# Kernel tuning notes

Measured on AMD Instinct MI355X. Metric: run time of the kernel, lower is better.

## Reference

```python
import jax, jax.numpy as jnp
import numpy as np

F = 26            # number of categorical fields
V_FIELD = 8000    # vocab per field
V = F * V_FIELD   # 208000, size of every shared-index table
D_EMB = 16
DNN_IN = F * F * D_EMB  # 10816
H1, H2 = 256, 128
BS = 4096
NUM_DENSE = 13
EPS = 1e-5


def setup_inputs() -> dict:
    key = jax.random.key(0)
    ks = jax.random.split(key, 16)
    def n(k, shape, s=0.05):
        return jax.random.normal(k, shape, dtype=jnp.float32) * s
    return {
        "X_sparse": jax.random.randint(ks[0], (BS, F), 0, V_FIELD, dtype=jnp.int32),
        "X_dense": jax.random.normal(ks[1], (BS, NUM_DENSE), dtype=jnp.float32),
        "fm1_emb": n(ks[2], (V, 1)),
        "bias": jnp.zeros((1,), jnp.float32),
        "fm1_dense_W": n(ks[3], (1, NUM_DENSE)),
        "fm1_dense_b": jnp.zeros((1,), jnp.float32),
        "emb_tables": n(ks[4], (F, V, D_EMB)),  # one table per field (FFM)
        "dense_W": n(ks[5], (DNN_IN, NUM_DENSE)),
        "dense_b": jnp.zeros((DNN_IN,), jnp.float32),
        "W1": n(ks[6], (H1, DNN_IN)),
        "b1": jnp.zeros((H1,), jnp.float32),
        "g1": jnp.ones((H1,), jnp.float32),
        "beta1": jnp.zeros((H1,), jnp.float32),
        "W2": n(ks[7], (H2, H1)),
        "b2": jnp.zeros((H2,), jnp.float32),
        "g2": jnp.ones((H2,), jnp.float32),
        "beta2": jnp.zeros((H2,), jnp.float32),
        "Wout": n(ks[8], (1, H2)),
        "bout": jnp.zeros((1,), jnp.float32),
    }


def _bn(x, g, b):
    # BatchNorm1d in training mode: biased batch statistics
    m = jnp.mean(x, axis=0)
    v = jnp.var(x, axis=0)
    return (x - m) * jax.lax.rsqrt(v + EPS) * g + b


def reference(X_sparse, X_dense, fm1_emb, bias, fm1_dense_W, fm1_dense_b,
              emb_tables, dense_W, dense_b,
              W1, b1, g1, beta1, W2, b2, g2, beta2, Wout, bout):
    offsets = (jnp.arange(F, dtype=X_sparse.dtype) * V_FIELD)[None, :]
    X = X_sparse + offsets                      # [bs, F] global indices

    # FM first order
    fm1 = jnp.sum(fm1_emb[X], axis=1) + bias    # [bs, 1]
    fm1 = fm1 + X_dense @ fm1_dense_W.T + fm1_dense_b

    # FFM second order: E[t, b, f, d] = table t looked up at field f's index
    E = emb_tables[:, X, :]                     # [F, bs, F, d]
    A = jnp.transpose(E, (1, 0, 2, 3))          # [bs, F_table, F_field, d]
    # pair (i<j): xs[j][:, i] * xs[i][:, j] = A[b, i, j] * A[b, j, i]
    P = A * jnp.swapaxes(A, 1, 2)               # [bs, F, F, d]
    mask = jnp.triu(jnp.ones((F, F), jnp.float32), 1)
    fm2 = jnp.einsum('bijd,ij->b', P, mask)[:, None]  # [bs, 1]

    # DNN: concat per-table lookups then flatten -> [bs, F*F*d]
    dnn = A.reshape(A.shape[0], DNN_IN)
    dnn = dnn + jax.nn.relu(X_dense @ dense_W.T + dense_b)
    h = jax.nn.relu(_bn(dnn @ W1.T + b1, g1, beta1))  # dropout is identity (eval)
    h = jax.nn.relu(_bn(h @ W2.T + b2, g2, beta2))
    out = h @ Wout.T + bout
    return jax.nn.sigmoid(fm1 + fm2 + out)
```

## Files before the change

### kernel.cpp

```cpp
#include <hip/hip_runtime.h>

typedef __bf16 bf16x8 __attribute__((ext_vector_type(8)));
typedef float f32x4 __attribute__((ext_vector_type(4)));

#define F_FIELDS 26
#define V_FIELD  8000
#define V_TOT    208000
#define D_EMBD   16
#define DNN_IN   10816
#define BS       4096
#define ND       13
#define H1_DIM   256
#define H2_DIM   128
#define NP1      8

__device__ __forceinline__ unsigned short f2bf(float f) {
  unsigned u = __float_as_uint(f);
  u += 0x7fffu + ((u >> 16) & 1u);
  return (unsigned short)(u >> 16);
}
__device__ __forceinline__ float bf2f(unsigned short h) {
  return __uint_as_float(((unsigned)h) << 16);
}
__device__ __forceinline__ float bflo(unsigned u) { return __uint_as_float(u << 16); }
__device__ __forceinline__ float bfhi(unsigned u) { return __uint_as_float(u & 0xffff0000u); }

__device__ __forceinline__ void gload16(const void* g, void* l) {
  __builtin_amdgcn_global_load_lds(
      (const __attribute__((address_space(1))) unsigned int*)g,
      (__attribute__((address_space(3))) unsigned int*)l, 16, 0, 0);
}

__device__ __forceinline__ float dot8bf(uint4 a, uint4 b) {
  const unsigned* pa = (const unsigned*)&a;
  const unsigned* pb = (const unsigned*)&b;
  float s = 0.f;
#pragma unroll
  for (int k = 0; k < 4; ++k)
    s += bflo(pa[k]) * bflo(pb[k]) + bfhi(pa[k]) * bfhi(pb[k]);
  return s;
}

__global__ __launch_bounds__(256) void k_gather(
    const int* __restrict__ Xs, const float* __restrict__ emb,
    const float* __restrict__ fm1_emb, const float* __restrict__ bias,
    const float* __restrict__ fm1dW, const float* __restrict__ fm1db,
    const float* __restrict__ Xd,
    const float* __restrict__ W1, const float* __restrict__ W2,
    const float* __restrict__ dW, const float* __restrict__ db_,
    unsigned short* __restrict__ W1b, unsigned short* __restrict__ W2b,
    unsigned short* __restrict__ dWb,
    unsigned short* __restrict__ Abf, float* __restrict__ fm12) {
  const int b = blockIdx.x;
  const int tid = threadIdx.x;
  const int lane = tid & 63, wave = tid >> 6;
  __shared__ int   sidx[F_FIELDS];
  __shared__ float sc1[F_FIELDS];
  __shared__ __align__(16) unsigned short As[676 * 16];
  __shared__ float wred[4];

  if (tid < F_FIELDS) {
    int v = Xs[b * F_FIELDS + tid] + tid * V_FIELD;
    sidx[tid] = v;
    sc1[tid] = fm1_emb[v];
  }
  __syncthreads();

  const int q = tid & 3, rbase = tid >> 2;
  float4 vv[11];
#pragma unroll
  for (int it = 0; it < 11; ++it) {
    int r = rbase + it * 64;
    if (r < 676) {
      int i = r / 26, j = r - i * 26;
      const float* src = emb + ((size_t)i * V_TOT + sidx[j]) * D_EMBD + q * 4;
      vv[it] = *(const float4*)src;
    }
  }
  const int n1 = H1_DIM * DNN_IN, n2 = H2_DIM * H1_DIM;
  for (int t = b * 256 + tid; t < n1 + n2; t += BS * 256) {
    if (t < n1) W1b[t] = f2bf(W1[t]);
    else        W2b[t - n1] = f2bf(W2[t - n1]);
  }
  for (int e = b * 256 + tid; e < DNN_IN; e += BS * 256) {
    unsigned short row[32];
#pragma unroll
    for (int k = 0; k < 13; ++k) row[k] = f2bf(dW[e * 13 + k]);
    row[13] = f2bf(db_[e]);
#pragma unroll
    for (int k = 14; k < 32; ++k) row[k] = 0;
#pragma unroll
    for (int k = 0; k < 32; ++k) dWb[e * 32 + k] = row[k];
  }
#pragma unroll
  for (int it = 0; it < 11; ++it) {
    int r = rbase + it * 64;
    if (r < 676) {
      ushort4 u;
      u.x = f2bf(vv[it].x); u.y = f2bf(vv[it].y);
      u.z = f2bf(vv[it].z); u.w = f2bf(vv[it].w);
      *(ushort4*)&As[r * 16 + q * 4] = u;
      *(ushort4*)&Abf[(size_t)b * DNN_IN + r * 16 + q * 4] = u;
    }
  }
  __syncthreads();

  float acc2 = 0.f;
  for (int p = tid; p < 325; p += 256) {
    float disc = sqrtf((float)(2601 - 8 * p));
    int i = (int)((51.f - disc) * 0.5f);
    int cum = 25 * i - ((i * (i - 1)) >> 1);
    int j = i + 1 + (p - cum);
    const unsigned short* r1 = &As[(i * 26 + j) * 16];
    const unsigned short* r2 = &As[(j * 26 + i) * 16];
    acc2 += dot8bf(*(const uint4*)r1, *(const uint4*)r2);
    acc2 += dot8bf(*(const uint4*)(r1 + 8), *(const uint4*)(r2 + 8));
  }
#pragma unroll
  for (int off = 32; off; off >>= 1) acc2 += __shfl_down(acc2, off);
  if (lane == 0) wred[wave] = acc2;
  __syncthreads();
  if (tid == 0) {
    float fm2 = wred[0] + wred[1] + wred[2] + wred[3];
    float f1 = bias[0] + fm1db[0];
#pragma unroll
    for (int j = 0; j < F_FIELDS; ++j) f1 += sc1[j];
    for (int k = 0; k < ND; ++k) f1 += Xd[b * ND + k] * fm1dW[k];
    fm12[b] = f1 + fm2;
  }
}

__global__ __launch_bounds__(256) void k_gemm1(
    const unsigned short* __restrict__ A, const unsigned short* __restrict__ B,
    const unsigned short* __restrict__ dWb, const float* __restrict__ Xd,
    float* __restrict__ C) {
  __shared__ __align__(16) unsigned short sA[3][64 * 32];
  __shared__ __align__(16) unsigned short sB[3][256 * 32];
  __shared__ __align__(16) unsigned short sWd[3][1024];
  __shared__ __align__(16) unsigned short sD[64 * 32];
  __shared__ __align__(16) unsigned short sXd[64 * 32];
  const int tid = threadIdx.x;
  const int lane = tid & 63, w = tid >> 6;
  const int id = blockIdx.x;
  const int p = id & 7, mt = id >> 3;
  const int m0 = mt * 64;
  const int s0 = (338 * p) >> 3, s1 = (338 * (p + 1)) >> 3;
  C += (size_t)p * ((size_t)BS * H1_DIM);

  if (tid < 64) {
    const float* xr = Xd + (size_t)(m0 + tid) * ND;
    unsigned short row[32];
#pragma unroll
    for (int k = 0; k < 13; ++k) row[k] = f2bf(xr[k]);
    row[13] = 0x3F80;
#pragma unroll
    for (int k = 14; k < 32; ++k) row[k] = 0;
#pragma unroll
    for (int k = 0; k < 32; ++k) sXd[tid * 32 + k] = row[k];
  }
  __syncthreads();

  const int q = tid & 3, rr = tid >> 2;
  const unsigned short* gA  = A + (size_t)(m0 + rr) * DNN_IN + q * 8;
  const unsigned short* gB0 = B + (size_t)rr * DNN_IN + q * 8;
  const int fr = lane & 15, fk = lane >> 4;
  const int oA = fr * 32 + fk * 8;
  const int oB = (w * 64 + fr) * 32 + fk * 8;

  const bf16x8 avd = *(const bf16x8*)&sXd[(w * 16 + fr) * 32 + fk * 8];
  const int oW0 = fr * 32 + fk * 8;
  const int oW1 = (16 + fr) * 32 + fk * 8;
  const int drow = w * 16 + fk * 4;

  f32x4 acc[4][4] = {};
  const f32x4 zf = {0.f, 0.f, 0.f, 0.f};

#define STAGE1(ks, bi) do { const int ko_ = (ks) * 32;                      \
    gload16(gA + ko_, &sA[bi][tid * 8]);                                    \
    gload16(gB0 + ko_, &sB[bi][tid * 8]);                                   \
    gload16(gB0 + (size_t)64 * DNN_IN + ko_, &sB[bi][2048 + tid * 8]);      \
    gload16(gB0 + (size_t)128 * DNN_IN + ko_, &sB[bi][4096 + tid * 8]);     \
    gload16(gB0 + (size_t)192 * DNN_IN + ko_, &sB[bi][6144 + tid * 8]);     \
    gload16(dWb + (size_t)ko_ * 32 + (size_t)lane * 8, &sWd[bi][lane * 8]); \
    gload16(dWb + (size_t)ko_ * 32 + 512 + (size_t)lane * 8,                \
            &sWd[bi][512 + lane * 8]); } while (0)

  STAGE1(s0, 0);
  if (s0 + 1 < s1) STAGE1(s0 + 1, 1);
  if (s0 + 2 < s1) STAGE1(s0 + 2, 2);

  int bi = 0;
  for (int ks = s0; ks < s1; ++ks) {
    if (ks + 2 < s1)      asm volatile("s_waitcnt vmcnt(14)" ::: "memory");
    else if (ks + 1 < s1) asm volatile("s_waitcnt vmcnt(7)" ::: "memory");
    else                  asm volatile("s_waitcnt vmcnt(0)" ::: "memory");
    __builtin_amdgcn_sched_barrier(0);
    __builtin_amdgcn_s_barrier();
    bf16x8 bw0 = *(const bf16x8*)&sWd[bi][oW0];
    bf16x8 bw1 = *(const bf16x8*)&sWd[bi][oW1];
    bf16x8 av[4], bv[4];
#pragma unroll
    for (int mi = 0; mi < 4; ++mi) av[mi] = *(const bf16x8*)&sA[bi][oA + mi * 512];
#pragma unroll
    for (int ni = 0; ni < 4; ++ni) bv[ni] = *(const bf16x8*)&sB[bi][oB + ni * 512];
    asm volatile("s_waitcnt lgkmcnt(0)" ::: "memory");
    __builtin_amdgcn_sched_barrier(0);
    f32x4 d0 = __builtin_amdgcn_mfma_f32_16x16x32_bf16(avd, bw0, zf, 0, 0, 0);
    f32x4 d1 = __builtin_amdgcn_mfma_f32_16x16x32_bf16(avd, bw1, zf, 0, 0, 0);
#pragma unroll
    for (int mi = 0; mi < 4; ++mi)
#pragma unroll
      for (int ni = 0; ni < 4; ++ni)
        acc[mi][ni] = __builtin_amdgcn_mfma_f32_16x16x32_bf16(
            av[mi], bv[ni], acc[mi][ni], 0, 0, 0);
#pragma unroll
    for (int r = 0; r < 4; ++r) {
      sD[(drow + r) * 32 + fr]      = f2bf(fmaxf(d0[r], 0.f));
      sD[(drow + r) * 32 + 16 + fr] = f2bf(fmaxf(d1[r], 0.f));
    }
    asm volatile("s_waitcnt lgkmcnt(0)" ::: "memory");
    __builtin_amdgcn_sched_barrier(0);
    __builtin_amdgcn_s_barrier();
    if (ks + 3 < s1) STAGE1(ks + 3, bi);
    bf16x8 dv[4];
#pragma unroll
    for (int mi = 0; mi < 4; ++mi) dv[mi] = *(const bf16x8*)&sD[oA + mi * 512];
    asm volatile("s_waitcnt lgkmcnt(0)" ::: "memory");
    __builtin_amdgcn_sched_barrier(0);
#pragma unroll
    for (int mi = 0; mi < 4; ++mi)
#pragma unroll
      for (int ni = 0; ni < 4; ++ni)
        acc[mi][ni] = __builtin_amdgcn_mfma_f32_16x16x32_bf16(
            dv[mi], bv[ni], acc[mi][ni], 0, 0, 0);
    bi = bi + 1; if (bi == 3) bi = 0;
  }
#pragma unroll
  for (int mi = 0; mi < 4; ++mi)
#pragma unroll
    for (int ni = 0; ni < 4; ++ni)
#pragma unroll
      for (int r = 0; r < 4; ++r) {
        int row = m0 + mi * 16 + fk * 4 + r;
        int col = w * 64 + ni * 16 + fr;
        C[(size_t)row * H1_DIM + col] = acc[mi][ni][r];
      }
#undef STAGE1
}

__global__ __launch_bounds__(256) void k_stat1(
    const float* __restrict__ Yp, const float* __restrict__ b1,
    float* __restrict__ Y1, float* __restrict__ ps, float* __restrict__ pq) {
  const int g = blockIdx.x, n = threadIdx.x;
  const size_t plane = (size_t)BS * H1_DIM;
  float s = 0.f, s2 = 0.f;
  float bn = b1[n];
  for (int bb = 0; bb < 16; ++bb) {
    size_t o = (size_t)(g * 16 + bb) * H1_DIM + n;
    float y = bn;
#pragma unroll
    for (int pp = 0; pp < NP1; ++pp) y += Yp[o + pp * plane];
    Y1[o] = y; s += y; s2 += y * y;
  }
  ps[g * H1_DIM + n] = s;
  pq[g * H1_DIM + n] = s2;
}

__global__ __launch_bounds__(256) void k_apply1(
    const float* __restrict__ Y1, const float* __restrict__ ps,
    const float* __restrict__ pq, const float* __restrict__ g1,
    const float* __restrict__ be1, unsigned short* __restrict__ H1b) {
  const int g = blockIdx.x, n = threadIdx.x;
  float s = 0.f, s2 = 0.f;
  for (int gg = 0; gg < 256; ++gg) {
    s += ps[gg * H1_DIM + n];
    s2 += pq[gg * H1_DIM + n];
  }
  float m = s * (1.f / BS);
  float v = s2 * (1.f / BS) - m * m;
  float r = rsqrtf(v + 1e-5f);
  float ga = g1[n], bb_ = be1[n];
  for (int bb = 0; bb < 16; ++bb) {
    size_t o = (size_t)(g * 16 + bb) * H1_DIM + n;
    float h = (Y1[o] - m) * r * ga + bb_;
    H1b[o] = f2bf(fmaxf(h, 0.f));
  }
}

__global__ __launch_bounds__(256) void k_gemm2(
    const unsigned short* __restrict__ A, const unsigned short* __restrict__ B,
    const float* __restrict__ b2, float* __restrict__ Y2,
    float* __restrict__ ps, float* __restrict__ pq) {
  __shared__ __align__(16) unsigned short sA[2][128 * 32];
  __shared__ __align__(16) unsigned short sB[2][128 * 32];
  __shared__ float redS[8][H2_DIM];
  __shared__ float redQ[8][H2_DIM];
  const int tid = threadIdx.x;
  const int lane = tid & 63, wave = tid >> 6;
  const int m0 = blockIdx.x * 128;

  const int q = tid & 3, rr = tid >> 2;
  const unsigned short* gA0 = A + (size_t)(m0 + rr) * H1_DIM + q * 8;
  const unsigned short* gA1 = gA0 + (size_t)64 * H1_DIM;
  const unsigned short* gB0 = B + (size_t)rr * H1_DIM + q * 8;
  const unsigned short* gB1 = gB0 + (size_t)64 * H1_DIM;
  const int lo = wave * 512;

  const int wr = wave >> 1, wc = wave & 1;
  const int fr = lane & 15, fk = lane >> 4;
  const int oA = (wr * 64 + fr) * 32 + fk * 8;
  const int oB = (wc * 64 + fr) * 32 + fk * 8;

  f32x4 acc[4][4] = {};
  {
    gload16(gA0, &sA[0][lo]);
    gload16(gA1, &sA[0][2048 + lo]);
    gload16(gB0, &sB[0][lo]);
    gload16(gB1, &sB[0][2048 + lo]);
  }
  for (int ks = 0; ks < 8; ++ks) {
    const int cur = ks & 1;
    if (ks + 1 < 8) {
      const int ko = (ks + 1) * 32;
      gload16(gA0 + ko, &sA[cur ^ 1][lo]);
      gload16(gA1 + ko, &sA[cur ^ 1][2048 + lo]);
      gload16(gB0 + ko, &sB[cur ^ 1][lo]);
      gload16(gB1 + ko, &sB[cur ^ 1][2048 + lo]);
      asm volatile("s_waitcnt vmcnt(4)" ::: "memory");
    } else {
      asm volatile("s_waitcnt vmcnt(0)" ::: "memory");
    }
    __builtin_amdgcn_sched_barrier(0);
    __builtin_amdgcn_s_barrier();
    bf16x8 av[4], bv[4];
#pragma unroll
    for (int mi = 0; mi < 4; ++mi) av[mi] = *(const bf16x8*)&sA[cur][oA + mi * 512];
#pragma unroll
    for (int ni = 0; ni < 4; ++ni) bv[ni] = *(const bf16x8*)&sB[cur][oB + ni * 512];
    asm volatile("s_waitcnt lgkmcnt(0)" ::: "memory");
    __builtin_amdgcn_sched_barrier(0);
    __builtin_amdgcn_s_barrier();
#pragma unroll
    for (int mi = 0; mi < 4; ++mi)
#pragma unroll
      for (int ni = 0; ni < 4; ++ni)
        acc[mi][ni] = __builtin_amdgcn_mfma_f32_16x16x32_bf16(
            av[mi], bv[ni], acc[mi][ni], 0, 0, 0);
  }
  float sc[4] = {0.f, 0.f, 0.f, 0.f}, sq[4] = {0.f, 0.f, 0.f, 0.f};
#pragma unroll
  for (int ni = 0; ni < 4; ++ni) {
    int col = wc * 64 + ni * 16 + fr;
    float bcol = b2[col];
#pragma unroll
    for (int mi = 0; mi < 4; ++mi)
#pragma unroll
      for (int r = 0; r < 4; ++r) {
        int row = m0 + wr * 64 + mi * 16 + fk * 4 + r;
        float y = acc[mi][ni][r] + bcol;
        Y2[(size_t)row * H2_DIM + col] = y;
        sc[ni] += y; sq[ni] += y * y;
      }
  }
  const int slot = wr * 4 + fk;
#pragma unroll
  for (int ni = 0; ni < 4; ++ni) {
    int col = wc * 64 + ni * 16 + fr;
    redS[slot][col] = sc[ni];
    redQ[slot][col] = sq[ni];
  }
  __syncthreads();
  if (tid < H2_DIM) {
    float s = 0.f, s2 = 0.f;
#pragma unroll
    for (int sl = 0; sl < 8; ++sl) { s += redS[sl][tid]; s2 += redQ[sl][tid]; }
    ps[blockIdx.x * H2_DIM + tid] = s;
    pq[blockIdx.x * H2_DIM + tid] = s2;
  }
}

__global__ __launch_bounds__(256) void k_final(
    const float* __restrict__ Y2, const float* __restrict__ ps,
    const float* __restrict__ pq, const float* __restrict__ g2,
    const float* __restrict__ be2, const float* __restrict__ Wout,
    const float* __restrict__ bout, const float* __restrict__ fm12,
    float* __restrict__ out) {
  const int tid = threadIdx.x, wave = tid >> 6, lane = tid & 63;
  __shared__ float sm[H2_DIM], sr[H2_DIM], sg[H2_DIM], sbe[H2_DIM], sw[H2_DIM];
  if (tid < H2_DIM) {
    float s = 0.f, s2 = 0.f;
    for (int g = 0; g < 32; ++g) {
      s += ps[g * H2_DIM + tid];
      s2 += pq[g * H2_DIM + tid];
    }
    float m = s * (1.f / BS);
    float v = s2 * (1.f / BS) - m * m;
    sm[tid] = m; sr[tid] = rsqrtf(v + 1e-5f);
    sg[tid] = g2[tid]; sbe[tid] = be2[tid]; sw[tid] = Wout[tid];
  }
  __syncthreads();
  const float bo = bout[0];
  for (int ii = 0; ii < 16; ++ii) {
    int s = blockIdx.x * 64 + wave * 16 + ii;
    float acc = 0.f;
#pragma unroll
    for (int nn = 0; nn < 2; ++nn) {
      int n = lane + nn * 64;
      float y = Y2[(size_t)s * H2_DIM + n];
      float h = (y - sm[n]) * sr[n] * sg[n] + sbe[n];
      acc += fmaxf(h, 0.f) * sw[n];
    }
#pragma unroll
    for (int off = 32; off; off >>= 1) acc += __shfl_down(acc, off);
    if (lane == 0) {
      float logit = fm12[s] + acc + bo;
      out[s] = 1.f / (1.f + expf(-logit));
    }
  }
}

extern "C" void kernel_launch(void* const* d_in, const int* in_sizes, int n_in,
                              void* d_out, int out_size, void* d_ws, size_t ws_size,
                              hipStream_t stream) {
  const int*   Xs     = (const int*)d_in[0];
  const float* Xd     = (const float*)d_in[1];
  const float* fm1e   = (const float*)d_in[2];
  const float* bias   = (const float*)d_in[3];
  const float* fm1dW  = (const float*)d_in[4];
  const float* fm1db  = (const float*)d_in[5];
  const float* emb    = (const float*)d_in[6];
  const float* dW     = (const float*)d_in[7];
  const float* db_    = (const float*)d_in[8];
  const float* W1     = (const float*)d_in[9];
  const float* b1     = (const float*)d_in[10];
  const float* g1     = (const float*)d_in[11];
  const float* be1    = (const float*)d_in[12];
  const float* W2     = (const float*)d_in[13];
  const float* b2     = (const float*)d_in[14];
  const float* g2     = (const float*)d_in[15];
  const float* be2    = (const float*)d_in[16];
  const float* Wout   = (const float*)d_in[17];
  const float* bout   = (const float*)d_in[18];
  float* out = (float*)d_out;

  char* w = (char*)d_ws;
  unsigned short* Dnn = (unsigned short*)w; w += (size_t)BS * DNN_IN * 2;
  unsigned short* W1b = (unsigned short*)w; w += (size_t)H1_DIM * DNN_IN * 2;
  unsigned short* W2b = (unsigned short*)w; w += (size_t)H2_DIM * H1_DIM * 2;
  unsigned short* dWb = (unsigned short*)w; w += (size_t)DNN_IN * 32 * 2;
  float* fm12 = (float*)w;  w += (size_t)BS * 4;
  float* Ypart = (float*)w; w += (size_t)NP1 * BS * H1_DIM * 4;
  float* Y1 = (float*)w;    w += (size_t)BS * H1_DIM * 4;
  unsigned short* H1b = (unsigned short*)w; w += (size_t)BS * H1_DIM * 2;
  float* Y2 = (float*)w;    w += (size_t)BS * H2_DIM * 4;
  float* ps1 = (float*)w;   w += 256 * H1_DIM * 4;
  float* pq1 = (float*)w;   w += 256 * H1_DIM * 4;
  float* ps2 = (float*)w;   w += 32 * H2_DIM * 4;
  float* pq2 = (float*)w;   w += 32 * H2_DIM * 4;

  k_gather<<<BS, 256, 0, stream>>>(Xs, emb, fm1e, bias, fm1dW, fm1db, Xd,
                                   W1, W2, dW, db_, W1b, W2b, dWb, Dnn, fm12);
  k_gemm1<<<64 * NP1, 256, 0, stream>>>(Dnn, W1b, dWb, Xd, Ypart);
  k_stat1<<<256, 256, 0, stream>>>(Ypart, b1, Y1, ps1, pq1);
  k_apply1<<<256, 256, 0, stream>>>(Y1, ps1, pq1, g1, be1, H1b);
  k_gemm2<<<32, 256, 0, stream>>>(H1b, W2b, b2, Y2, ps2, pq2);
  k_final<<<BS / 64, 256, 0, stream>>>(Y2, ps2, pq2, g2, be2, Wout, bout, fm12, out);
}
```

Baseline: 187.1 us.

## Fuse dense-feature add into A tile before MFMA and store split-K partials as bf16

The GEMM1 main loop now computes the relu(Xd·dW) dense term with swapped MFMA operands so each lane owns contiguous columns, adds it to the gathered embedding tile, and writes the sum back to LDS as bf16. A single set of 16 MFMAs on the combined operand replaces the two sets previously issued per k-step. The split-K partial outputs are also written as bf16 instead of fp32, halving the partial-sum traffic read by the stats kernel. In exchange, the rounding of the A+dense sum and of the partial results to bf16 costs some accuracy.

Result: no change. 183.7 us (-1.8%).

```diff
diff --git a/kernel.cpp b/kernel.cpp
--- a/kernel.cpp
+++ b/kernel.cpp
@@ -24,6 +24,9 @@
 }
 __device__ __forceinline__ float bflo(unsigned u) { return __uint_as_float(u << 16); }
 __device__ __forceinline__ float bfhi(unsigned u) { return __uint_as_float(u & 0xffff0000u); }
+__device__ __forceinline__ unsigned packbf(float a, float b) {
+  return (unsigned)f2bf(a) | ((unsigned)f2bf(b) << 16);
+}
 
 __device__ __forceinline__ void gload16(const void* g, void* l) {
   __builtin_amdgcn_global_load_lds(
@@ -133,7 +136,7 @@
 __global__ __launch_bounds__(256) void k_gemm1(
     const unsigned short* __restrict__ A, const unsigned short* __restrict__ B,
     const unsigned short* __restrict__ dWb, const float* __restrict__ Xd,
-    float* __restrict__ C) {
+    unsigned short* __restrict__ C) {
   __shared__ __align__(16) unsigned short sA[3][64 * 32];
   __shared__ __align__(16) unsigned short sB[3][256 * 32];
   __shared__ __align__(16) unsigned short sWd[3][1024];
@@ -167,10 +170,9 @@
   const int oA = fr * 32 + fk * 8;
   const int oB = (w * 64 + fr) * 32 + fk * 8;
 
-  const bf16x8 avd = *(const bf16x8*)&sXd[(w * 16 + fr) * 32 + fk * 8];
-  const int oW0 = fr * 32 + fk * 8;
-  const int oW1 = (16 + fr) * 32 + fk * 8;
-  const int drow = w * 16 + fk * 4;
+  const bf16x8 bvd = *(const bf16x8*)&sXd[(w * 16 + fr) * 32 + fk * 8];
+  const int erow = (w * 16 + fr) * 32;
+  const int ecol = fk * 4;
 
   f32x4 acc[4][4] = {};
   const f32x4 zf = {0.f, 0.f, 0.f, 0.f};
@@ -196,43 +198,39 @@
     else                  asm volatile("s_waitcnt vmcnt(0)" ::: "memory");
     __builtin_amdgcn_sched_barrier(0);
     __builtin_amdgcn_s_barrier();
-    bf16x8 bw0 = *(const bf16x8*)&sWd[bi][oW0];
-    bf16x8 bw1 = *(const bf16x8*)&sWd[bi][oW1];
-    bf16x8 av[4], bv[4];
-#pragma unroll
-    for (int mi = 0; mi < 4; ++mi) av[mi] = *(const bf16x8*)&sA[bi][oA + mi * 512];
+    bf16x8 aw0 = *(const bf16x8*)&sWd[bi][fr * 32 + fk * 8];
+    bf16x8 aw1 = *(const bf16x8*)&sWd[bi][(16 + fr) * 32 + fk * 8];
+    bf16x8 bv[4];
 #pragma unroll
     for (int ni = 0; ni < 4; ++ni) bv[ni] = *(const bf16x8*)&sB[bi][oB + ni * 512];
+    uint2 a0 = *(const uint2*)&sA[bi][erow + ecol];
+    uint2 a1 = *(const uint2*)&sA[bi][erow + 16 + ecol];
     asm volatile("s_waitcnt lgkmcnt(0)" ::: "memory");
     __builtin_amdgcn_sched_barrier(0);
-    f32x4 d0 = __builtin_amdgcn_mfma_f32_16x16x32_bf16(avd, bw0, zf, 0, 0, 0);
-    f32x4 d1 = __builtin_amdgcn_mfma_f32_16x16x32_bf16(avd, bw1, zf, 0, 0, 0);
+    f32x4 d0 = __builtin_amdgcn_mfma_f32_16x16x32_bf16(aw0, bvd, zf, 0, 0, 0);
+    f32x4 d1 = __builtin_amdgcn_mfma_f32_16x16x32_bf16(aw1, bvd, zf, 0, 0, 0);
+    uint2 e0, e1;
+    e0.x = packbf(bflo(a0.x) + fmaxf(d0[0], 0.f), bfhi(a0.x) + fmaxf(d0[1], 0.f));
+    e0.y = packbf(bflo(a0.y) + fmaxf(d0[2], 0.f), bfhi(a0.y) + fmaxf(d0[3], 0.f));
+    e1.x = packbf(bflo(a1.x) + fmaxf(d1[0], 0.f), bfhi(a1.x) + fmaxf(d1[1], 0.f));
+    e1.y = packbf(bflo(a1.y) + fmaxf(d1[2], 0.f), bfhi(a1.y) + fmaxf(d1[3], 0.f));
+    *(uint2*)&sD[erow + ecol] = e0;
+    *(uint2*)&sD[erow + 16 + ecol] = e1;
+    asm volatile("s_waitcnt lgkmcnt(0)" ::: "memory");
+    __builtin_amdgcn_sched_barrier(0);
+    __builtin_amdgcn_s_barrier();
+    if (ks + 3 < s1) STAGE1(ks + 3, bi);
+    bf16x8 ev[4];
+#pragma unroll
+    for (int mi = 0; mi < 4; ++mi) ev[mi] = *(const bf16x8*)&sD[oA + mi * 512];
+    asm volatile("s_waitcnt lgkmcnt(0)" ::: "memory");
+    __builtin_amdgcn_sched_barrier(0);
 #pragma unroll
     for (int mi = 0; mi < 4; ++mi)
 #pragma unroll
       for (int ni = 0; ni < 4; ++ni)
         acc[mi][ni] = __builtin_amdgcn_mfma_f32_16x16x32_bf16(
-            av[mi], bv[ni], acc[mi][ni], 0, 0, 0);
-#pragma unroll
-    for (int r = 0; r < 4; ++r) {
-      sD[(drow + r) * 32 + fr]      = f2bf(fmaxf(d0[r], 0.f));
-      sD[(drow + r) * 32 + 16 + fr] = f2bf(fmaxf(d1[r], 0.f));
-    }
-    asm volatile("s_waitcnt lgkmcnt(0)" ::: "memory");
-    __builtin_amdgcn_sched_barrier(0);
-    __builtin_amdgcn_s_barrier();
-    if (ks + 3 < s1) STAGE1(ks + 3, bi);
-    bf16x8 dv[4];
-#pragma unroll
-    for (int mi = 0; mi < 4; ++mi) dv[mi] = *(const bf16x8*)&sD[oA + mi * 512];
-    asm volatile("s_waitcnt lgkmcnt(0)" ::: "memory");
-    __builtin_amdgcn_sched_barrier(0);
-#pragma unroll
-    for (int mi = 0; mi < 4; ++mi)
-#pragma unroll
-      for (int ni = 0; ni < 4; ++ni)
-        acc[mi][ni] = __builtin_amdgcn_mfma_f32_16x16x32_bf16(
-            dv[mi], bv[ni], acc[mi][ni], 0, 0, 0);
+            ev[mi], bv[ni], acc[mi][ni], 0, 0, 0);
     bi = bi + 1; if (bi == 3) bi = 0;
   }
 #pragma unroll
@@ -243,13 +241,13 @@
       for (int r = 0; r < 4; ++r) {
         int row = m0 + mi * 16 + fk * 4 + r;
         int col = w * 64 + ni * 16 + fr;
-        C[(size_t)row * H1_DIM + col] = acc[mi][ni][r];
+        C[(size_t)row * H1_DIM + col] = f2bf(acc[mi][ni][r]);
       }
 #undef STAGE1
 }
 
 __global__ __launch_bounds__(256) void k_stat1(
-    const float* __restrict__ Yp, const float* __restrict__ b1,
+    const unsigned short* __restrict__ Yp, const float* __restrict__ b1,
     float* __restrict__ Y1, float* __restrict__ ps, float* __restrict__ pq) {
   const int g = blockIdx.x, n = threadIdx.x;
   const size_t plane = (size_t)BS * H1_DIM;
@@ -259,7 +257,7 @@
     size_t o = (size_t)(g * 16 + bb) * H1_DIM + n;
     float y = bn;
 #pragma unroll
-    for (int pp = 0; pp < NP1; ++pp) y += Yp[o + pp * plane];
+    for (int pp = 0; pp < NP1; ++pp) y += bf2f(Yp[o + pp * plane]);
     Y1[o] = y; s += y; s2 += y * y;
   }
   ps[g * H1_DIM + n] = s;
@@ -449,7 +447,7 @@
   unsigned short* W2b = (unsigned short*)w; w += (size_t)H2_DIM * H1_DIM * 2;
   unsigned short* dWb = (unsigned short*)w; w += (size_t)DNN_IN * 32 * 2;
   float* fm12 = (float*)w;  w += (size_t)BS * 4;
-  float* Ypart = (float*)w; w += (size_t)NP1 * BS * H1_DIM * 4;
+  unsigned short* Ypart = (unsigned short*)w; w += (size_t)NP1 * BS * H1_DIM * 2;
   float* Y1 = (float*)w;    w += (size_t)BS * H1_DIM * 4;
   unsigned short* H1b = (unsigned short*)w; w += (size_t)BS * H1_DIM * 2;
   float* Y2 = (float*)w;    w += (size_t)BS * H2_DIM * 4;
```
